# Kernel tuning notes

Measured on AMD Instinct MI355X. Metric: run time of the kernel, lower is better.

Reference implementation:

```python
import jax, jax.numpy as jnp
import numpy as np

B, N, E, H = 8, 2000, 20, 128


def setup_inputs() -> dict:
    key = jax.random.key(0)
    ks = jax.random.split(key, 9)
    s = 1.0 / np.sqrt(H)
    return {
        "x": jax.random.normal(ks[0], (B, N, H), dtype=jnp.float32),
        "e": jax.random.normal(ks[1], (B, N * E, H), dtype=jnp.float32),
        "Wu": jax.random.uniform(ks[2], (H, H), jnp.float32, -s, s),
        "bu": jax.random.uniform(ks[3], (H,), jnp.float32, -s, s),
        "Wv": jax.random.uniform(ks[4], (H, H), jnp.float32, -s, s),
        "bv": jax.random.uniform(ks[5], (H,), jnp.float32, -s, s),
        "We": jax.random.uniform(ks[6], (H, H), jnp.float32, -s, s),
        "be": jax.random.uniform(ks[7], (H,), jnp.float32, -s, s),
        "edge_index": jax.random.randint(ks[8], (B, N * E), 0, N, dtype=jnp.int32),
        "n_edges": E,
    }


def reference(x, e, Wu, bu, Wv, bv, We, be, edge_index, n_edges):
    b, n, h = x.shape
    Ux = x @ Wu + bu                      # [B, N, H] node self-embedding
    Vx = x @ Wv + bv                      # [B, N, H] neighbor embedding
    Ve = e @ We + be                      # [B, N*E, H] edge embedding
    # softmax over the n_edges axis per (node, channel)
    Ve = jax.nn.softmax(Ve.reshape(b, n, n_edges, h), axis=2)
    # gather neighbor features along node axis via edge_index
    Vx_g = jnp.take_along_axis(Vx, edge_index[..., None], axis=1)  # [B, N*E, H]
    to = (Ve * Vx_g.reshape(b, n, n_edges, h)).sum(axis=2)          # [B, N, H]
    return Ux + to
```

## Files before the change

### kernel.cpp

```cpp
#include <hip/hip_runtime.h>

#define B_   8
#define NN   2000
#define EE   20
#define HH   128
#define BN   (B_*NN)
#define NE   (NN*EE)

typedef unsigned short ushort_t;
typedef __bf16 bf16x8 __attribute__((ext_vector_type(8)));
typedef float  f32x4  __attribute__((ext_vector_type(4)));
typedef float  f4     __attribute__((ext_vector_type(4)));
typedef unsigned short us8 __attribute__((ext_vector_type(8)));
typedef unsigned short us4 __attribute__((ext_vector_type(4)));

union FragU { us8 u; bf16x8 b; };

__device__ __forceinline__ float b2f(ushort_t v) {
    union { unsigned int i; float f; } c; c.i = ((unsigned int)v) << 16; return c.f;
}
__device__ __forceinline__ ushort_t f2b(float f) {
    union { float f; unsigned int i; } c; c.f = f;
    unsigned int r = (c.i + 0x7FFFu + ((c.i >> 16) & 1u)) >> 16;
    return (ushort_t)r;
}

__global__ __launch_bounds__(256) void k1_embed(
    const float* __restrict__ x,
    const float* __restrict__ Wu, const float* __restrict__ bu,
    const float* __restrict__ Wv, const float* __restrict__ bv,
    ushort_t* __restrict__ Uxb, ushort_t* __restrict__ Vxb)
{
    const int tid  = threadIdx.x;
    const int lane = tid & 63;
    const int wave = tid >> 6;
    const int wm = wave >> 1, wn = wave & 1;
    const int q  = lane >> 4, ln = lane & 15;
    const int m0 = blockIdx.x * 64;
    const int sel = blockIdx.y;
    const float* W    = sel ? Wv : Wu;
    const float* bias = sel ? bv : bu;
    ushort_t* dst = sel ? Vxb : Uxb;

    FragU af[2][4];
#pragma unroll
    for (int tm = 0; tm < 2; ++tm)
#pragma unroll
        for (int ki = 0; ki < 4; ++ki) {
            const float* p = x + (size_t)(m0 + wm * 32 + tm * 16 + ln) * HH + ki * 32 + q * 8;
            f4 lo = *(const f4*)(p);
            f4 hi = *(const f4*)(p + 4);
            us8 t;
#pragma unroll
            for (int r = 0; r < 4; ++r) { t[r] = f2b(lo[r]); t[r + 4] = f2b(hi[r]); }
            af[tm][ki].u = t;
        }

    FragU bf[4][4];
#pragma unroll
    for (int ki = 0; ki < 4; ++ki)
#pragma unroll
        for (int tn = 0; tn < 4; ++tn) {
            int n = wn * 64 + tn * 16 + ln;
            us8 t;
#pragma unroll
            for (int i = 0; i < 8; ++i) t[i] = f2b(W[(ki * 32 + q * 8 + i) * HH + n]);
            bf[ki][tn].u = t;
        }

    f32x4 acc[2][4];
#pragma unroll
    for (int tm = 0; tm < 2; ++tm)
#pragma unroll
        for (int tn = 0; tn < 4; ++tn) acc[tm][tn] = (f32x4){0.f, 0.f, 0.f, 0.f};

#pragma unroll
    for (int ki = 0; ki < 4; ++ki)
#pragma unroll
        for (int tm = 0; tm < 2; ++tm)
#pragma unroll
            for (int tn = 0; tn < 4; ++tn)
                acc[tm][tn] = __builtin_amdgcn_mfma_f32_16x16x32_bf16(
                    af[tm][ki].b, bf[ki][tn].b, acc[tm][tn], 0, 0, 0);

#pragma unroll
    for (int tn = 0; tn < 4; ++tn) {
        int col = wn * 64 + tn * 16 + ln;
        float bb = bias[col];
#pragma unroll
        for (int tm = 0; tm < 2; ++tm) {
            int rowb = m0 + wm * 32 + tm * 16 + q * 4;
#pragma unroll
            for (int r = 0; r < 4; ++r)
                dst[(size_t)(rowb + r) * HH + col] = f2b(acc[tm][tn][r] + bb);
        }
    }
}

#define ASTR 136
#define CSTR 84

__global__ __launch_bounds__(256, 4) void k2_fused(
    const float* __restrict__ e, const float* __restrict__ We,
    const int* __restrict__ eidx,
    const ushort_t* __restrict__ Uxb, const ushort_t* __restrict__ Vxb,
    float* __restrict__ out)
{
    __shared__ __align__(16) ushort_t smem[11008];
    __shared__ int sidx[80];

    const int tid  = threadIdx.x;
    const int lane = tid & 63;
    const int wave = tid >> 6;
    const int q  = lane >> 4, ln = lane & 15;

    const int b   = blockIdx.y;
    const int nl0 = blockIdx.x * 4;
    const size_t erow0 = (size_t)b * NE + (size_t)nl0 * EE;

    for (int c = tid; c < 80 * 32; c += 256) {
        int row = c >> 5, col = (c & 31) * 4;
        f4 v = *(const f4*)(e + (erow0 + row) * HH + col);
        us4 pk;
#pragma unroll
        for (int r = 0; r < 4; ++r) pk[r] = f2b(v[r]);
        *(us4*)(&smem[row * ASTR + col]) = pk;
    }
    if (tid < 80) sidx[tid] = eidx[erow0 + tid];

    FragU bf[4][2];
#pragma unroll
    for (int ki = 0; ki < 4; ++ki)
#pragma unroll
        for (int tn = 0; tn < 2; ++tn) {
            int n = wave * 32 + tn * 16 + ln;
            us8 t;
#pragma unroll
            for (int i = 0; i < 8; ++i) t[i] = f2b(We[(ki * 32 + q * 8 + i) * HH + n]);
            bf[ki][tn].u = t;
        }

    f32x4 acc[5][2];
#pragma unroll
    for (int tm = 0; tm < 5; ++tm)
#pragma unroll
        for (int tn = 0; tn < 2; ++tn) acc[tm][tn] = (f32x4){0.f, 0.f, 0.f, 0.f};

    __syncthreads();

#pragma unroll
    for (int ki = 0; ki < 4; ++ki) {
        FragU af[5];
#pragma unroll
        for (int tm = 0; tm < 5; ++tm)
            af[tm].u = *(const us8*)(&smem[(tm * 16 + ln) * ASTR + ki * 32 + q * 8]);
#pragma unroll
        for (int tm = 0; tm < 5; ++tm)
#pragma unroll
            for (int tn = 0; tn < 2; ++tn)
                acc[tm][tn] = __builtin_amdgcn_mfma_f32_16x16x32_bf16(
                    af[tm].b, bf[ki][tn].b, acc[tm][tn], 0, 0, 0);
    }

    __syncthreads();

#pragma unroll
    for (int tm = 0; tm < 5; ++tm)
#pragma unroll
        for (int tn = 0; tn < 2; ++tn) {
            int col  = wave * 32 + tn * 16 + ln;
            int rowb = tm * 16 + q * 4;
            us4 pk;
#pragma unroll
            for (int r = 0; r < 4; ++r) pk[r] = f2b(acc[tm][tn][r]);
            *(us4*)(&smem[col * CSTR + rowb]) = pk;
        }

    __syncthreads();

    const int h  = tid & 127;
    const int gp = tid >> 7;
#pragma unroll 1
    for (int j = 0; j < 2; ++j) {
        int g = gp + 2 * j;
        const ushort_t* ctp = &smem[h * CSTR + g * 20];
        float lv[20];
#pragma unroll
        for (int i = 0; i < 5; ++i) {
            us4 v = *(const us4*)(ctp + i * 4);
#pragma unroll
            for (int r = 0; r < 4; ++r) lv[i * 4 + r] = b2f(v[r]);
        }
        float mx = lv[0];
#pragma unroll
        for (int k = 1; k < EE; ++k) mx = fmaxf(mx, lv[k]);

        ushort_t gv[20];
        const int ib = g * 20;
#pragma unroll
        for (int k = 0; k < EE; ++k)
            gv[k] = Vxb[(size_t)(b * NN + sidx[ib + k]) * HH + h];

        float s = 0.f, a = 0.f;
#pragma unroll
        for (int k = 0; k < EE; ++k) {
            float p = __expf(lv[k] - mx);
            s += p;
            a = fmaf(p, b2f(gv[k]), a);
        }
        size_t orow = (size_t)(b * NN + nl0 + g) * HH + h;
        out[orow] = b2f(Uxb[orow]) + a / s;
    }
}

extern "C" void kernel_launch(void* const* d_in, const int* in_sizes, int n_in,
                              void* d_out, int out_size, void* d_ws, size_t ws_size,
                              hipStream_t stream) {
    const float* x  = (const float*)d_in[0];
    const float* e  = (const float*)d_in[1];
    const float* Wu = (const float*)d_in[2];
    const float* bu = (const float*)d_in[3];
    const float* Wv = (const float*)d_in[4];
    const float* bv = (const float*)d_in[5];
    const float* We = (const float*)d_in[6];
    const int*   eidx = (const int*)d_in[8];

    ushort_t* Uxb = (ushort_t*)d_ws;
    ushort_t* Vxb = (ushort_t*)((char*)d_ws + (size_t)BN * HH * 2);
    float*    o   = (float*)d_out;

    k1_embed<<<dim3(250, 2), 256, 0, stream>>>(x, Wu, bu, Wv, bv, Uxb, Vxb);
    k2_fused<<<dim3(500, 8), 256, 0, stream>>>(e, We, eidx, Uxb, Vxb, o);
}
```

Baseline: 279.4 us.

## Stream edge features into LDS via direct global-to-LDS loads with XOR swizzle

Edge-feature tiles are now copied from global memory straight into LDS as fp32 with global_load_lds, bypassing registers, and stored with an XOR-swizzled column layout to avoid bank conflicts. The bf16 conversion moves to fragment-load time using packed v_cvt_pk_bf16_f32 instructions. LDS usage grows from about 22KB to 40KB per block, which may cut the number of resident blocks per CU. The index load is moved after the GEMM and reuses the same shared buffer.

```diff
diff --git a/kernel.cpp b/kernel.cpp
--- a/kernel.cpp
+++ b/kernel.cpp
@@ -15,6 +15,7 @@
 typedef unsigned short us4 __attribute__((ext_vector_type(4)));
 
 union FragU { us8 u; bf16x8 b; };
+union Frag32 { unsigned int w[4]; us8 u; bf16x8 b; };
 
 __device__ __forceinline__ float b2f(ushort_t v) {
     union { unsigned int i; float f; } c; c.i = ((unsigned int)v) << 16; return c.f;
@@ -97,7 +98,6 @@
     }
 }
 
-#define ASTR 136
 #define CSTR 84
 
 __global__ __launch_bounds__(256, 4) void k2_fused(
@@ -106,8 +106,7 @@
     const ushort_t* __restrict__ Uxb, const ushort_t* __restrict__ Vxb,
     float* __restrict__ out)
 {
-    __shared__ __align__(16) ushort_t smem[11008];
-    __shared__ int sidx[80];
+    __shared__ __align__(16) unsigned char smem[40960];
 
     const int tid  = threadIdx.x;
     const int lane = tid & 63;
@@ -118,17 +117,23 @@
     const int nl0 = blockIdx.x * 4;
     const size_t erow0 = (size_t)b * NE + (size_t)nl0 * EE;
 
-    for (int c = tid; c < 80 * 32; c += 256) {
-        int row = c >> 5, col = (c & 31) * 4;
-        f4 v = *(const f4*)(e + (erow0 + row) * HH + col);
-        us4 pk;
-#pragma unroll
-        for (int r = 0; r < 4; ++r) pk[r] = f2b(v[r]);
-        *(us4*)(&smem[row * ASTR + col]) = pk;
-    }
-    if (tid < 80) sidx[tid] = eidx[erow0 + tid];
-
-    FragU bf[4][2];
+    {
+        const int rl = lane >> 5;
+        const int sl = lane & 31;
+#pragma unroll
+        for (int i = 0; i < 10; ++i) {
+            const int r0 = wave * 20 + 2 * i;
+            const int r  = r0 + rl;
+            const int ss = sl ^ (r & 7);
+            const float* gp = e + (erow0 + r) * (size_t)HH + (ss << 2);
+            __builtin_amdgcn_global_load_lds(
+                (const __attribute__((address_space(1))) void*)gp,
+                (__attribute__((address_space(3))) void*)(smem + r0 * 512),
+                16, 0, 0);
+        }
+    }
+
+    FragU bfr[4][2];
 #pragma unroll
     for (int ki = 0; ki < 4; ++ki)
 #pragma unroll
@@ -137,7 +142,7 @@
             us8 t;
 #pragma unroll
             for (int i = 0; i < 8; ++i) t[i] = f2b(We[(ki * 32 + q * 8 + i) * HH + n]);
-            bf[ki][tn].u = t;
+            bfr[ki][tn].u = t;
         }
 
     f32x4 acc[5][2];
@@ -146,24 +151,39 @@
 #pragma unroll
         for (int tn = 0; tn < 2; ++tn) acc[tm][tn] = (f32x4){0.f, 0.f, 0.f, 0.f};
 
+    asm volatile("s_waitcnt vmcnt(0)" ::: "memory");
     __syncthreads();
 
+    const float* As = (const float*)smem;
 #pragma unroll
     for (int ki = 0; ki < 4; ++ki) {
-        FragU af[5];
-#pragma unroll
-        for (int tm = 0; tm < 5; ++tm)
-            af[tm].u = *(const us8*)(&smem[(tm * 16 + ln) * ASTR + ki * 32 + q * 8]);
+        Frag32 af[5];
+#pragma unroll
+        for (int tm = 0; tm < 5; ++tm) {
+            const int r  = tm * 16 + ln;
+            const int sw = r & 7;
+            const int s0 = ki * 8 + q * 2;
+            f4 lo = *(const f4*)(As + r * 128 + ((s0    ) ^ sw) * 4);
+            f4 hi = *(const f4*)(As + r * 128 + ((s0 + 1) ^ sw) * 4);
+            asm("v_cvt_pk_bf16_f32 %0, %1, %2" : "=v"(af[tm].w[0]) : "v"(lo[0]), "v"(lo[1]));
+            asm("v_cvt_pk_bf16_f32 %0, %1, %2" : "=v"(af[tm].w[1]) : "v"(lo[2]), "v"(lo[3]));
+            asm("v_cvt_pk_bf16_f32 %0, %1, %2" : "=v"(af[tm].w[2]) : "v"(hi[0]), "v"(hi[1]));
+            asm("v_cvt_pk_bf16_f32 %0, %1, %2" : "=v"(af[tm].w[3]) : "v"(hi[2]), "v"(hi[3]));
+        }
 #pragma unroll
         for (int tm = 0; tm < 5; ++tm)
 #pragma unroll
             for (int tn = 0; tn < 2; ++tn)
                 acc[tm][tn] = __builtin_amdgcn_mfma_f32_16x16x32_bf16(
-                    af[tm].b, bf[ki][tn].b, acc[tm][tn], 0, 0, 0);
+                    af[tm].b, bfr[ki][tn].b, acc[tm][tn], 0, 0, 0);
     }
 
     __syncthreads();
 
+    int* sidx = (int*)(smem + 38400);
+    if (tid < 80) sidx[tid] = eidx[erow0 + tid];
+
+    ushort_t* CT = (ushort_t*)smem;
 #pragma unroll
     for (int tm = 0; tm < 5; ++tm)
 #pragma unroll
@@ -173,7 +193,7 @@
             us4 pk;
 #pragma unroll
             for (int r = 0; r < 4; ++r) pk[r] = f2b(acc[tm][tn][r]);
-            *(us4*)(&smem[col * CSTR + rowb]) = pk;
+            *(us4*)(&CT[col * CSTR + rowb]) = pk;
         }
 
     __syncthreads();
@@ -183,7 +203,7 @@
 #pragma unroll 1
     for (int j = 0; j < 2; ++j) {
         int g = gp + 2 * j;
-        const ushort_t* ctp = &smem[h * CSTR + g * 20];
+        const ushort_t* ctp = &CT[h * CSTR + g * 20];
         float lv[20];
 #pragma unroll
         for (int i = 0; i < 5; ++i) {
```

Measured after the change: 267.2 us. 4.4% less time.
